# Optimization experiments

Hardware: AMD Instinct MI355X
Metric: run time of the kernel (lower is better)

## Reference

```python
import jax, jax.numpy as jnp
import numpy as np

N, M, D = 16384, 1024, 1024


def setup_inputs() -> dict:
    key = jax.random.key(0)
    kq, kp = jax.random.split(key)
    query = jax.random.normal(kq, (N, D), dtype=jnp.float32)
    proto = jax.random.normal(kp, (M, D), dtype=jnp.float32)
    return {"query": query, "proto": proto}


def reference(query, proto):
    # Pairwise squared euclidean: ||q||^2 - 2 q.p + ||p||^2  (same math as
    # the expand+pow+sum in compute_euclidean, but without the [N,M,D] blowup).
    q2 = jnp.sum(query * query, axis=-1, keepdims=True)          # [N,1]
    p2 = jnp.sum(proto * proto, axis=-1)                          # [M]
    qp = jnp.einsum('nd,md->nm', query, proto)                    # [N,M]
    dists = q2 - 2.0 * qp + p2[None, :]                           # [N,M]
    # Original applies F.softmax(-dists, dim=1) (named log_p_y but is softmax).
    return jax.nn.softmax(-dists, axis=1)
```

## Files before the change

### kernel.cpp

```cpp
#include <hip/hip_runtime.h>
#include <stdint.h>

#define N_Q 16384
#define M_P 1024
#define D_K 1024

typedef __attribute__((ext_vector_type(8))) __bf16 bf16x8;
typedef __attribute__((ext_vector_type(4))) float floatx4;
typedef __attribute__((ext_vector_type(8))) unsigned short ushort8v;

#define AS1 __attribute__((address_space(1)))
#define AS3 __attribute__((address_space(3)))

__device__ __forceinline__ unsigned short f2bf(float f) {
    unsigned int u = __float_as_uint(f);
    u += 0x7fffu + ((u >> 16) & 1u);
    return (unsigned short)(u >> 16);
}
__device__ __forceinline__ float bf2f(unsigned short h) {
    return __uint_as_float(((unsigned int)h) << 16);
}

__global__ __launch_bounds__(256) void convert_all_kernel(
    const float* __restrict__ query, unsigned short* __restrict__ qh,
    unsigned short* __restrict__ ql, const float* __restrict__ proto,
    unsigned short* __restrict__ ph, unsigned short* __restrict__ pl,
    float* __restrict__ p2) {
    __shared__ float sred[4];
    int b = blockIdx.x;
    int t = threadIdx.x;
    if (b < 2048) {
        size_t base = (size_t)b * 1024 + t;
#pragma unroll
        for (int k = 0; k < 4; ++k) {
            size_t idx = base + (size_t)k * 256;
            const floatx4* src = (const floatx4*)query + idx * 2;
            floatx4 v0 = __builtin_nontemporal_load(src);
            floatx4 v1 = __builtin_nontemporal_load(src + 1);
            ushort8v h, l;
            h[0] = f2bf(v0.x); l[0] = f2bf(v0.x - bf2f(h[0]));
            h[1] = f2bf(v0.y); l[1] = f2bf(v0.y - bf2f(h[1]));
            h[2] = f2bf(v0.z); l[2] = f2bf(v0.z - bf2f(h[2]));
            h[3] = f2bf(v0.w); l[3] = f2bf(v0.w - bf2f(h[3]));
            h[4] = f2bf(v1.x); l[4] = f2bf(v1.x - bf2f(h[4]));
            h[5] = f2bf(v1.y); l[5] = f2bf(v1.y - bf2f(h[5]));
            h[6] = f2bf(v1.z); l[6] = f2bf(v1.z - bf2f(h[6]));
            h[7] = f2bf(v1.w); l[7] = f2bf(v1.w - bf2f(h[7]));
            ((ushort8v*)qh)[idx] = h;
            ((ushort8v*)ql)[idx] = l;
        }
    } else {
        int m = b - 2048;
        size_t base4 = (size_t)m * (D_K / 4) + t;
        float4 v = ((const float4*)proto)[base4];
        ushort4 h, l;
        h.x = f2bf(v.x); l.x = f2bf(v.x - bf2f(h.x));
        h.y = f2bf(v.y); l.y = f2bf(v.y - bf2f(h.y));
        h.z = f2bf(v.z); l.z = f2bf(v.z - bf2f(h.z));
        h.w = f2bf(v.w); l.w = f2bf(v.w - bf2f(h.w));
        ((ushort4*)ph)[base4] = h;
        ((ushort4*)pl)[base4] = l;
        float sq = v.x * v.x + v.y * v.y + v.z * v.z + v.w * v.w;
#pragma unroll
        for (int off = 1; off < 64; off <<= 1) sq += __shfl_xor(sq, off);
        if ((t & 63) == 0) sred[t >> 6] = sq;
        __syncthreads();
        if (t == 0) p2[m] = sred[0] + sred[1] + sred[2] + sred[3];
    }
}

__global__ __launch_bounds__(256, 3) void gemm_logits_kernel(
    const unsigned short* __restrict__ qh, const unsigned short* __restrict__ ql,
    const unsigned short* __restrict__ ph, const unsigned short* __restrict__ pl,
    const float* __restrict__ p2, float* __restrict__ out) {
    __shared__ unsigned short lds[4 * 128 * 32];

    const int tid = threadIdx.x;
    const int wave = tid >> 6;
    const int lane = tid & 63;
    const int nt = blockIdx.x & 127;
    const int mt = blockIdx.x >> 7;
    const int row0 = nt * 128;
    const int col0 = mt * 128;

    unsigned short* sAh = lds;
    unsigned short* sAl = lds + 4096;
    unsigned short* sBh = lds + 8192;
    unsigned short* sBl = lds + 12288;

    const unsigned short* gsrc;
    unsigned short* ldst;
    int grow0;
    if (wave == 0)      { gsrc = qh; grow0 = row0; ldst = sAh; }
    else if (wave == 1) { gsrc = ql; grow0 = row0; ldst = sAl; }
    else if (wave == 2) { gsrc = ph; grow0 = col0; ldst = sBh; }
    else                { gsrc = pl; grow0 = col0; ldst = sBl; }

    const int rl = lane >> 2;
    const int cio = (lane & 3) ^ ((lane >> 3) & 3);
    const unsigned short* gbase = gsrc + (size_t)(grow0 + rl) * D_K + cio * 8;

    floatx4 zero = {0.0f, 0.0f, 0.0f, 0.0f};
    floatx4 acc[4][4];
#pragma unroll
    for (int i = 0; i < 4; ++i)
#pragma unroll
        for (int j = 0; j < 4; ++j) acc[i][j] = zero;

    const int wrow = (wave & 1) * 64;
    const int wcol = (wave >> 1) * 64;
    const int rsel = lane & 15;
    const int kq = lane >> 4;
    const int sA0 = (wrow >> 4);
    const int sB0 = (wcol >> 4);
    const int gsw = 4 * rsel + (kq ^ ((rsel >> 1) & 3));
    const int fragoff = gsw * 8;

    for (int kt = 0; kt < D_K / 32; ++kt) {
#pragma unroll
        for (int i = 0; i < 8; ++i) {
            const unsigned short* gp = gbase + (size_t)i * 16 * D_K + kt * 32;
            __builtin_amdgcn_global_load_lds(
                (const AS1 unsigned int*)(const void*)gp,
                (AS3 unsigned int*)(void*)(ldst + i * 512), 16, 0, 0);
        }
        __syncthreads();

        bf16x8 ah[4], al[4], bh[4], bl[4];
#pragma unroll
        for (int i = 0; i < 4; ++i) {
            const int aoff = (sA0 + i) * 512 + fragoff;
            ah[i] = *(const bf16x8*)(sAh + aoff);
            al[i] = *(const bf16x8*)(sAl + aoff);
            const int boff = (sB0 + i) * 512 + fragoff;
            bh[i] = *(const bf16x8*)(sBh + boff);
            bl[i] = *(const bf16x8*)(sBl + boff);
        }

#pragma unroll
        for (int i = 0; i < 4; ++i)
#pragma unroll
            for (int j = 0; j < 4; ++j) {
                acc[i][j] = __builtin_amdgcn_mfma_f32_16x16x32_bf16(ah[i], bh[j], acc[i][j], 0, 0, 0);
                acc[i][j] = __builtin_amdgcn_mfma_f32_16x16x32_bf16(ah[i], bl[j], acc[i][j], 0, 0, 0);
                acc[i][j] = __builtin_amdgcn_mfma_f32_16x16x32_bf16(al[i], bh[j], acc[i][j], 0, 0, 0);
            }
        __syncthreads();
    }

#pragma unroll
    for (int j = 0; j < 4; ++j) {
        const int gc = col0 + wcol + j * 16 + rsel;
        const float p2v = p2[gc];
#pragma unroll
        for (int i = 0; i < 4; ++i) {
            const int gr = row0 + wrow + i * 16 + kq * 4;
#pragma unroll
            for (int r = 0; r < 4; ++r) {
                out[(size_t)(gr + r) * M_P + gc] = 2.0f * acc[i][j][r] - p2v;
            }
        }
    }
}

__global__ __launch_bounds__(256) void naive_logits_kernel(
    const float* __restrict__ query, const float* __restrict__ proto,
    float* __restrict__ out) {
    __shared__ float qs[D_K];
    int n = blockIdx.x;
    int t = threadIdx.x;
    ((float4*)qs)[t] = ((const float4*)(query + (size_t)n * D_K))[t];
    __syncthreads();
    float acc[4] = {0.f, 0.f, 0.f, 0.f};
    float pp[4] = {0.f, 0.f, 0.f, 0.f};
    for (int d = 0; d < D_K; d += 4) {
        float4 qv = *(const float4*)(qs + d);
#pragma unroll
        for (int j = 0; j < 4; ++j) {
            const float4 pv = *(const float4*)(proto + (size_t)(t + 256 * j) * D_K + d);
            acc[j] += qv.x * pv.x + qv.y * pv.y + qv.z * pv.z + qv.w * pv.w;
            pp[j] += pv.x * pv.x + pv.y * pv.y + pv.z * pv.z + pv.w * pv.w;
        }
    }
#pragma unroll
    for (int j = 0; j < 4; ++j)
        out[(size_t)n * M_P + t + 256 * j] = 2.0f * acc[j] - pp[j];
}

__global__ __launch_bounds__(256) void softmax_kernel(float* __restrict__ out) {
    const int lane = threadIdx.x & 63;
    int n = blockIdx.x * 4 + (threadIdx.x >> 6);
    for (int it = 0; it < 2; ++it, n += 8192) {
        float* row = out + (size_t)n * M_P;
        floatx4 v[4];
#pragma unroll
        for (int k = 0; k < 4; ++k)
            v[k] = *((const floatx4*)(row + k * 256) + lane);
        float mx = fmaxf(fmaxf(v[0].x, v[0].y), fmaxf(v[0].z, v[0].w));
#pragma unroll
        for (int k = 1; k < 4; ++k)
            mx = fmaxf(mx, fmaxf(fmaxf(v[k].x, v[k].y), fmaxf(v[k].z, v[k].w)));
#pragma unroll
        for (int off = 1; off < 64; off <<= 1) mx = fmaxf(mx, __shfl_xor(mx, off));
        float s = 0.0f;
#pragma unroll
        for (int k = 0; k < 4; ++k) {
            v[k].x = __expf(v[k].x - mx);
            v[k].y = __expf(v[k].y - mx);
            v[k].z = __expf(v[k].z - mx);
            v[k].w = __expf(v[k].w - mx);
            s += v[k].x + v[k].y + v[k].z + v[k].w;
        }
#pragma unroll
        for (int off = 1; off < 64; off <<= 1) s += __shfl_xor(s, off);
        const float inv = 1.0f / s;
#pragma unroll
        for (int k = 0; k < 4; ++k) {
            floatx4 o;
            o.x = v[k].x * inv; o.y = v[k].y * inv;
            o.z = v[k].z * inv; o.w = v[k].w * inv;
            __builtin_nontemporal_store(o, (floatx4*)(row + k * 256) + lane);
        }
    }
}

extern "C" void kernel_launch(void* const* d_in, const int* in_sizes, int n_in,
                              void* d_out, int out_size, void* d_ws, size_t ws_size,
                              hipStream_t stream) {
    const float* query = (const float*)d_in[0];
    const float* proto = (const float*)d_in[1];
    float* out = (float*)d_out;

    const size_t qElems = (size_t)N_Q * D_K;
    const size_t pElems = (size_t)M_P * D_K;
    const size_t needed = qElems * 2 * 2 + pElems * 2 * 2 + M_P * 4;

    if (ws_size >= needed) {
        unsigned short* qh = (unsigned short*)d_ws;
        unsigned short* ql = qh + qElems;
        unsigned short* ph = ql + qElems;
        unsigned short* pl = ph + pElems;
        float* p2 = (float*)(pl + pElems);

        convert_all_kernel<<<2048 + M_P, 256, 0, stream>>>(
            query, qh, ql, proto, ph, pl, p2);
        gemm_logits_kernel<<<(N_Q / 128) * (M_P / 128), 256, 0, stream>>>(
            qh, ql, ph, pl, p2, out);
    } else {
        naive_logits_kernel<<<N_Q, 256, 0, stream>>>(query, proto, out);
    }
    softmax_kernel<<<2048, 256, 0, stream>>>(out);
}
```

Before: 231.8 us.

## Fuse softmax into GEMM with full-row 32x1024 tiles per block

Replaces the 128x128-tiled logits GEMM and the separate softmax pass with one kernel. Each 512-thread block computes a full 32-row by 1024-column strip in two passes over prototype halves, then does the row max, exp, sum and normalize in registers and shared memory before writing with nontemporal stores. This removes the round trip of the logits matrix through global memory. In exchange, arithmetic intensity per block is much lower: 32 rows of A against all 1024 prototypes means B is re-streamed for every block. It also holds larger accumulator state, which may hurt occupancy.

```diff
diff --git a/kernel.cpp b/kernel.cpp
--- a/kernel.cpp
+++ b/kernel.cpp
@@ -69,98 +69,199 @@
     }
 }
 
-__global__ __launch_bounds__(256, 3) void gemm_logits_kernel(
+__global__ __launch_bounds__(512, 4) void fused_gemm_softmax_kernel(
     const unsigned short* __restrict__ qh, const unsigned short* __restrict__ ql,
     const unsigned short* __restrict__ ph, const unsigned short* __restrict__ pl,
     const float* __restrict__ p2, float* __restrict__ out) {
-    __shared__ unsigned short lds[4 * 128 * 32];
+    __shared__ unsigned short sA[2 * 1024];
+    __shared__ unsigned short sB[2 * 16384];
+    __shared__ float wred[8 * 32];
+    __shared__ float wsum[8 * 32];
 
     const int tid = threadIdx.x;
     const int wave = tid >> 6;
     const int lane = tid & 63;
-    const int nt = blockIdx.x & 127;
-    const int mt = blockIdx.x >> 7;
-    const int row0 = nt * 128;
-    const int col0 = mt * 128;
-
-    unsigned short* sAh = lds;
-    unsigned short* sAl = lds + 4096;
-    unsigned short* sBh = lds + 8192;
-    unsigned short* sBl = lds + 12288;
-
-    const unsigned short* gsrc;
-    unsigned short* ldst;
-    int grow0;
-    if (wave == 0)      { gsrc = qh; grow0 = row0; ldst = sAh; }
-    else if (wave == 1) { gsrc = ql; grow0 = row0; ldst = sAl; }
-    else if (wave == 2) { gsrc = ph; grow0 = col0; ldst = sBh; }
-    else                { gsrc = pl; grow0 = col0; ldst = sBl; }
+    const int row0 = blockIdx.x * 32;
 
     const int rl = lane >> 2;
     const int cio = (lane & 3) ^ ((lane >> 3) & 3);
-    const unsigned short* gbase = gsrc + (size_t)(grow0 + rl) * D_K + cio * 8;
-
-    floatx4 zero = {0.0f, 0.0f, 0.0f, 0.0f};
-    floatx4 acc[4][4];
-#pragma unroll
-    for (int i = 0; i < 4; ++i)
-#pragma unroll
-        for (int j = 0; j < 4; ++j) acc[i][j] = zero;
-
-    const int wrow = (wave & 1) * 64;
-    const int wcol = (wave >> 1) * 64;
+    const size_t laneoff = (size_t)rl * D_K + cio * 8;
+
     const int rsel = lane & 15;
     const int kq = lane >> 4;
-    const int sA0 = (wrow >> 4);
-    const int sB0 = (wcol >> 4);
     const int gsw = 4 * rsel + (kq ^ ((rsel >> 1) & 3));
     const int fragoff = gsw * 8;
 
-    for (int kt = 0; kt < D_K / 32; ++kt) {
-#pragma unroll
-        for (int i = 0; i < 8; ++i) {
-            const unsigned short* gp = gbase + (size_t)i * 16 * D_K + kt * 32;
-            __builtin_amdgcn_global_load_lds(
-                (const AS1 unsigned int*)(const void*)gp,
-                (AS3 unsigned int*)(void*)(ldst + i * 512), 16, 0, 0);
-        }
-        __syncthreads();
-
-        bf16x8 ah[4], al[4], bh[4], bl[4];
-#pragma unroll
-        for (int i = 0; i < 4; ++i) {
-            const int aoff = (sA0 + i) * 512 + fragoff;
-            ah[i] = *(const bf16x8*)(sAh + aoff);
-            al[i] = *(const bf16x8*)(sAl + aoff);
-            const int boff = (sB0 + i) * 512 + fragoff;
-            bh[i] = *(const bf16x8*)(sBh + boff);
-            bl[i] = *(const bf16x8*)(sBl + boff);
-        }
-
-#pragma unroll
-        for (int i = 0; i < 4; ++i)
+    floatx4 zero = {0.0f, 0.0f, 0.0f, 0.0f};
+    floatx4 acc[2][2][4];
+#pragma unroll
+    for (int p = 0; p < 2; ++p)
+#pragma unroll
+        for (int i = 0; i < 2; ++i)
+#pragma unroll
+            for (int j = 0; j < 4; ++j) acc[p][i][j] = zero;
+
+#pragma unroll
+    for (int pass = 0; pass < 2; ++pass) {
+#pragma unroll 1
+        for (int kt = 0; kt < D_K / 32; ++kt) {
+            const int kbase = kt * 32;
+#pragma unroll
+            for (int u = 0; u < 4; ++u) {
+                const int s = wave * 4 + u;
+                const size_t goff = (size_t)(pass * 512 + s * 16) * D_K + kbase + laneoff;
+                __builtin_amdgcn_global_load_lds(
+                    (const AS1 unsigned int*)(const void*)(ph + goff),
+                    (AS3 unsigned int*)(void*)(sB + s * 512), 16, 0, 0);
+                __builtin_amdgcn_global_load_lds(
+                    (const AS1 unsigned int*)(const void*)(pl + goff),
+                    (AS3 unsigned int*)(void*)(sB + 16384 + s * 512), 16, 0, 0);
+            }
+            if (wave < 4) {
+                const unsigned short* gsrc = (wave < 2) ? qh : ql;
+                const int s = wave & 1;
+                const size_t goff = (size_t)(row0 + s * 16) * D_K + kbase + laneoff;
+                __builtin_amdgcn_global_load_lds(
+                    (const AS1 unsigned int*)(const void*)(gsrc + goff),
+                    (AS3 unsigned int*)(void*)(sA + (wave < 2 ? 0 : 1024) + s * 512),
+                    16, 0, 0);
+            }
+            __syncthreads();
+
+            bf16x8 ah[2], al[2];
+#pragma unroll
+            for (int i = 0; i < 2; ++i) {
+                ah[i] = *(const bf16x8*)(sA + i * 512 + fragoff);
+                al[i] = *(const bf16x8*)(sA + 1024 + i * 512 + fragoff);
+            }
 #pragma unroll
             for (int j = 0; j < 4; ++j) {
-                acc[i][j] = __builtin_amdgcn_mfma_f32_16x16x32_bf16(ah[i], bh[j], acc[i][j], 0, 0, 0);
-                acc[i][j] = __builtin_amdgcn_mfma_f32_16x16x32_bf16(ah[i], bl[j], acc[i][j], 0, 0, 0);
-                acc[i][j] = __builtin_amdgcn_mfma_f32_16x16x32_bf16(al[i], bh[j], acc[i][j], 0, 0, 0);
+                const int sj = wave * 4 + j;
+                bf16x8 bhj = *(const bf16x8*)(sB + sj * 512 + fragoff);
+                bf16x8 blj = *(const bf16x8*)(sB + 16384 + sj * 512 + fragoff);
+#pragma unroll
+                for (int i = 0; i < 2; ++i) {
+                    acc[pass][i][j] = __builtin_amdgcn_mfma_f32_16x16x32_bf16(ah[i], bhj, acc[pass][i][j], 0, 0, 0);
+                    acc[pass][i][j] = __builtin_amdgcn_mfma_f32_16x16x32_bf16(ah[i], blj, acc[pass][i][j], 0, 0, 0);
+                    acc[pass][i][j] = __builtin_amdgcn_mfma_f32_16x16x32_bf16(al[i], bhj, acc[pass][i][j], 0, 0, 0);
+                }
             }
-        __syncthreads();
-    }
-
-#pragma unroll
-    for (int j = 0; j < 4; ++j) {
-        const int gc = col0 + wcol + j * 16 + rsel;
-        const float p2v = p2[gc];
-#pragma unroll
-        for (int i = 0; i < 4; ++i) {
-            const int gr = row0 + wrow + i * 16 + kq * 4;
-#pragma unroll
-            for (int r = 0; r < 4; ++r) {
-                out[(size_t)(gr + r) * M_P + gc] = 2.0f * acc[i][j][r] - p2v;
-            }
-        }
-    }
+            __syncthreads();
+        }
+    }
+
+    float p2v[2][4];
+#pragma unroll
+    for (int p = 0; p < 2; ++p)
+#pragma unroll
+        for (int j = 0; j < 4; ++j)
+            p2v[p][j] = p2[p * 512 + wave * 64 + j * 16 + rsel];
+#pragma unroll
+    for (int p = 0; p < 2; ++p)
+#pragma unroll
+        for (int i = 0; i < 2; ++i)
+#pragma unroll
+            for (int j = 0; j < 4; ++j)
+#pragma unroll
+                for (int r = 0; r < 4; ++r)
+                    acc[p][i][j][r] = 2.0f * acc[p][i][j][r] - p2v[p][j];
+
+    float rmax[2][4];
+#pragma unroll
+    for (int i = 0; i < 2; ++i)
+#pragma unroll
+        for (int r = 0; r < 4; ++r) {
+            float m = acc[0][i][0][r];
+#pragma unroll
+            for (int p = 0; p < 2; ++p)
+#pragma unroll
+                for (int j = 0; j < 4; ++j) m = fmaxf(m, acc[p][i][j][r]);
+            rmax[i][r] = m;
+        }
+#pragma unroll
+    for (int off = 1; off < 16; off <<= 1)
+#pragma unroll
+        for (int i = 0; i < 2; ++i)
+#pragma unroll
+            for (int r = 0; r < 4; ++r)
+                rmax[i][r] = fmaxf(rmax[i][r], __shfl_xor(rmax[i][r], off));
+    if (rsel == 0) {
+#pragma unroll
+        for (int i = 0; i < 2; ++i)
+#pragma unroll
+            for (int r = 0; r < 4; ++r)
+                wred[wave * 32 + i * 16 + kq * 4 + r] = rmax[i][r];
+    }
+    __syncthreads();
+#pragma unroll
+    for (int i = 0; i < 2; ++i)
+#pragma unroll
+        for (int r = 0; r < 4; ++r) {
+            const int lr = i * 16 + kq * 4 + r;
+            float m = wred[lr];
+#pragma unroll
+            for (int w = 1; w < 8; ++w) m = fmaxf(m, wred[w * 32 + lr]);
+            rmax[i][r] = m;
+        }
+
+    float rsum[2][4];
+#pragma unroll
+    for (int i = 0; i < 2; ++i)
+#pragma unroll
+        for (int r = 0; r < 4; ++r) rsum[i][r] = 0.0f;
+#pragma unroll
+    for (int p = 0; p < 2; ++p)
+#pragma unroll
+        for (int i = 0; i < 2; ++i)
+#pragma unroll
+            for (int j = 0; j < 4; ++j)
+#pragma unroll
+                for (int r = 0; r < 4; ++r) {
+                    float e = __expf(acc[p][i][j][r] - rmax[i][r]);
+                    acc[p][i][j][r] = e;
+                    rsum[i][r] += e;
+                }
+#pragma unroll
+    for (int off = 1; off < 16; off <<= 1)
+#pragma unroll
+        for (int i = 0; i < 2; ++i)
+#pragma unroll
+            for (int r = 0; r < 4; ++r)
+                rsum[i][r] += __shfl_xor(rsum[i][r], off);
+    if (rsel == 0) {
+#pragma unroll
+        for (int i = 0; i < 2; ++i)
+#pragma unroll
+            for (int r = 0; r < 4; ++r)
+                wsum[wave * 32 + i * 16 + kq * 4 + r] = rsum[i][r];
+    }
+    __syncthreads();
+    float inv[2][4];
+#pragma unroll
+    for (int i = 0; i < 2; ++i)
+#pragma unroll
+        for (int r = 0; r < 4; ++r) {
+            const int lr = i * 16 + kq * 4 + r;
+            float s = wsum[lr];
+#pragma unroll
+            for (int w = 1; w < 8; ++w) s += wsum[w * 32 + lr];
+            inv[i][r] = 1.0f / s;
+        }
+
+#pragma unroll
+    for (int p = 0; p < 2; ++p)
+#pragma unroll
+        for (int j = 0; j < 4; ++j) {
+            const int gc = p * 512 + wave * 64 + j * 16 + rsel;
+#pragma unroll
+            for (int i = 0; i < 2; ++i)
+#pragma unroll
+                for (int r = 0; r < 4; ++r) {
+                    const int gr = row0 + i * 16 + kq * 4 + r;
+                    __builtin_nontemporal_store(acc[p][i][j][r] * inv[i][r],
+                                                &out[(size_t)gr * M_P + gc]);
+                }
+        }
 }
 
 __global__ __launch_bounds__(256) void naive_logits_kernel(
@@ -244,10 +345,10 @@
 
         convert_all_kernel<<<2048 + M_P, 256, 0, stream>>>(
             query, qh, ql, proto, ph, pl, p2);
-        gemm_logits_kernel<<<(N_Q / 128) * (M_P / 128), 256, 0, stream>>>(
+        fused_gemm_softmax_kernel<<<N_Q / 32, 512, 0, stream>>>(
             qh, ql, ph, pl, p2, out);
     } else {
         naive_logits_kernel<<<N_Q, 256, 0, stream>>>(query, proto, out);
-    }
-    softmax_kernel<<<2048, 256, 0, stream>>>(out);
-}
+        softmax_kernel<<<2048, 256, 0, stream>>>(out);
+    }
+}
```

After: 305.8 us. +31.9%, slower.

## Use two-wave 128x128 GEMM tiles with 64x128 per-wave output and grouped block order

Applied to the files above, without the earlier changes.

Shrinks the GEMM block from four waves to two, so each wave computes a 64x128 sub-tile with acc[4][8] and each wave loads both hi and lo halves of one operand. B fragments are loaded per column inside the MFMA loop, which means fewer LDS fragment reads per MFMA. The block index is remapped into groups of 8 row tiles by 8 column tiles to improve L2 reuse. The trade-off is more accumulator registers per wave and fewer waves per block, which can reduce latency hiding.

```diff
diff --git a/kernel.cpp b/kernel.cpp
--- a/kernel.cpp
+++ b/kernel.cpp
@@ -69,7 +69,7 @@
     }
 }
 
-__global__ __launch_bounds__(256, 3) void gemm_logits_kernel(
+__global__ __launch_bounds__(128, 2) void gemm_logits_kernel(
     const unsigned short* __restrict__ qh, const unsigned short* __restrict__ ql,
     const unsigned short* __restrict__ ph, const unsigned short* __restrict__ pl,
     const float* __restrict__ p2, float* __restrict__ out) {
@@ -78,8 +78,9 @@
     const int tid = threadIdx.x;
     const int wave = tid >> 6;
     const int lane = tid & 63;
-    const int nt = blockIdx.x & 127;
-    const int mt = blockIdx.x >> 7;
+    const int b = blockIdx.x;
+    const int mt = (b >> 3) & 7;
+    const int nt = (b & 7) | ((b >> 6) << 3);
     const int row0 = nt * 128;
     const int col0 = mt * 128;
 
@@ -88,73 +89,73 @@
     unsigned short* sBh = lds + 8192;
     unsigned short* sBl = lds + 12288;
 
-    const unsigned short* gsrc;
-    unsigned short* ldst;
-    int grow0;
-    if (wave == 0)      { gsrc = qh; grow0 = row0; ldst = sAh; }
-    else if (wave == 1) { gsrc = ql; grow0 = row0; ldst = sAl; }
-    else if (wave == 2) { gsrc = ph; grow0 = col0; ldst = sBh; }
-    else                { gsrc = pl; grow0 = col0; ldst = sBl; }
+    const unsigned short* gh = (wave == 0) ? qh : ph;
+    const unsigned short* gl = (wave == 0) ? ql : pl;
+    const int grow0 = (wave == 0) ? row0 : col0;
+    unsigned short* dsth = (wave == 0) ? sAh : sBh;
+    unsigned short* dstl = (wave == 0) ? sAl : sBl;
 
     const int rl = lane >> 2;
     const int cio = (lane & 3) ^ ((lane >> 3) & 3);
-    const unsigned short* gbase = gsrc + (size_t)(grow0 + rl) * D_K + cio * 8;
+    const size_t laneoff = (size_t)rl * D_K + cio * 8;
+    const unsigned short* gbh = gh + (size_t)grow0 * D_K + laneoff;
+    const unsigned short* gbl = gl + (size_t)grow0 * D_K + laneoff;
 
     floatx4 zero = {0.0f, 0.0f, 0.0f, 0.0f};
-    floatx4 acc[4][4];
+    floatx4 acc[4][8];
 #pragma unroll
     for (int i = 0; i < 4; ++i)
 #pragma unroll
-        for (int j = 0; j < 4; ++j) acc[i][j] = zero;
-
-    const int wrow = (wave & 1) * 64;
-    const int wcol = (wave >> 1) * 64;
+        for (int j = 0; j < 8; ++j) acc[i][j] = zero;
+
     const int rsel = lane & 15;
     const int kq = lane >> 4;
-    const int sA0 = (wrow >> 4);
-    const int sB0 = (wcol >> 4);
     const int gsw = 4 * rsel + (kq ^ ((rsel >> 1) & 3));
     const int fragoff = gsw * 8;
 
     for (int kt = 0; kt < D_K / 32; ++kt) {
-#pragma unroll
-        for (int i = 0; i < 8; ++i) {
-            const unsigned short* gp = gbase + (size_t)i * 16 * D_K + kt * 32;
+        const int kbase = kt * 32;
+#pragma unroll
+        for (int s = 0; s < 8; ++s) {
+            const size_t go = (size_t)(s * 16) * D_K + kbase;
             __builtin_amdgcn_global_load_lds(
-                (const AS1 unsigned int*)(const void*)gp,
-                (AS3 unsigned int*)(void*)(ldst + i * 512), 16, 0, 0);
+                (const AS1 unsigned int*)(const void*)(gbh + go),
+                (AS3 unsigned int*)(void*)(dsth + s * 512), 16, 0, 0);
+            __builtin_amdgcn_global_load_lds(
+                (const AS1 unsigned int*)(const void*)(gbl + go),
+                (AS3 unsigned int*)(void*)(dstl + s * 512), 16, 0, 0);
         }
         __syncthreads();
 
-        bf16x8 ah[4], al[4], bh[4], bl[4];
+        bf16x8 ah[4], al[4];
 #pragma unroll
         for (int i = 0; i < 4; ++i) {
-            const int aoff = (sA0 + i) * 512 + fragoff;
+            const int aoff = (wave * 4 + i) * 512 + fragoff;
             ah[i] = *(const bf16x8*)(sAh + aoff);
             al[i] = *(const bf16x8*)(sAl + aoff);
-            const int boff = (sB0 + i) * 512 + fragoff;
-            bh[i] = *(const bf16x8*)(sBh + boff);
-            bl[i] = *(const bf16x8*)(sBl + boff);
-        }
-
-#pragma unroll
-        for (int i = 0; i < 4; ++i)
-#pragma unroll
-            for (int j = 0; j < 4; ++j) {
-                acc[i][j] = __builtin_amdgcn_mfma_f32_16x16x32_bf16(ah[i], bh[j], acc[i][j], 0, 0, 0);
-                acc[i][j] = __builtin_amdgcn_mfma_f32_16x16x32_bf16(ah[i], bl[j], acc[i][j], 0, 0, 0);
-                acc[i][j] = __builtin_amdgcn_mfma_f32_16x16x32_bf16(al[i], bh[j], acc[i][j], 0, 0, 0);
+        }
+#pragma unroll
+        for (int j = 0; j < 8; ++j) {
+            const int boff = j * 512 + fragoff;
+            bf16x8 bhj = *(const bf16x8*)(sBh + boff);
+            bf16x8 blj = *(const bf16x8*)(sBl + boff);
+#pragma unroll
+            for (int i = 0; i < 4; ++i) {
+                acc[i][j] = __builtin_amdgcn_mfma_f32_16x16x32_bf16(ah[i], bhj, acc[i][j], 0, 0, 0);
+                acc[i][j] = __builtin_amdgcn_mfma_f32_16x16x32_bf16(ah[i], blj, acc[i][j], 0, 0, 0);
+                acc[i][j] = __builtin_amdgcn_mfma_f32_16x16x32_bf16(al[i], bhj, acc[i][j], 0, 0, 0);
             }
+        }
         __syncthreads();
     }
 
 #pragma unroll
-    for (int j = 0; j < 4; ++j) {
-        const int gc = col0 + wcol + j * 16 + rsel;
+    for (int j = 0; j < 8; ++j) {
+        const int gc = col0 + j * 16 + rsel;
         const float p2v = p2[gc];
 #pragma unroll
         for (int i = 0; i < 4; ++i) {
-            const int gr = row0 + wrow + i * 16 + kq * 4;
+            const int gr = row0 + wave * 64 + i * 16 + kq * 4;
 #pragma unroll
             for (int r = 0; r < 4; ++r) {
                 out[(size_t)(gr + r) * M_P + gc] = 2.0f * acc[i][j][r] - p2v;
@@ -244,7 +245,7 @@
 
         convert_all_kernel<<<2048 + M_P, 256, 0, stream>>>(
             query, qh, ql, proto, ph, pl, p2);
-        gemm_logits_kernel<<<(N_Q / 128) * (M_P / 128), 256, 0, stream>>>(
+        gemm_logits_kernel<<<(N_Q / 128) * (M_P / 128), 128, 0, stream>>>(
             qh, ql, ph, pl, p2, out);
     } else {
         naive_logits_kernel<<<N_Q, 256, 0, stream>>>(query, proto, out);
```

After: 229.9 us. Within noise of the previous version (-0.8%).
